# Optimization experiments

Hardware: AMD Instinct MI355X
Metric: run time of the kernel (lower is better)

The kernel has to match this reference:

```python
import jax, jax.numpy as jnp
import numpy as np

IN_FEATURES = 4096
OUT_FEATURES = 4096
SPARSITY = 0.99
NNZ = max(int(IN_FEATURES * OUT_FEATURES * (1.0 - SPARSITY)), 1)  # 167772
BATCH = 1024


def setup_inputs() -> dict:
    key = jax.random.key(0)
    kx, kv, kr, kc = jax.random.split(key, 4)
    x = jax.random.normal(kx, (BATCH, IN_FEATURES), dtype=jnp.float32)
    # values initialized ~ N(0,1) / sqrt(in_features), as in the module
    values = jax.random.normal(kv, (NNZ,), dtype=jnp.float32) * (1.0 / np.sqrt(IN_FEATURES))
    bias = jnp.zeros((OUT_FEATURES,), dtype=jnp.float32)
    rows = jax.random.randint(kr, (NNZ,), 0, IN_FEATURES)
    cols = jax.random.randint(kc, (NNZ,), 0, OUT_FEATURES)
    return {"x": x, "values": values, "bias": bias, "rows": rows, "cols": cols}


def reference(x, values, bias, rows, cols):
    # out = x @ W + bias, with sparse W(in,out) given in COO form.
    # torch's coalesce() sums duplicate (row,col) entries; scatter-add matches that.
    contrib = x[:, rows] * values  # [B, nnz]: gather input columns, scale by weights
    out = jnp.zeros((x.shape[0], OUT_FEATURES), dtype=x.dtype)
    out = out.at[:, cols].add(contrib)  # scatter-add into output columns
    return out + bias[None, :]
```

## Files before the change

kernel.cpp:

```cpp
#include <hip/hip_runtime.h>
#include <hip/hip_fp16.h>

#define BATCH 1024
#define IN_F 4096
#define OUT_F 4096
#define NCHUNK 8
#define CHUNK (BATCH / NCHUNK)
#define CAP 128

__global__ __launch_bounds__(256) void transpose_zero_k(const float* __restrict__ src,
                                                        __half* __restrict__ dst,
                                                        int R, int C,
                                                        int* __restrict__ cursor,
                                                        int4* __restrict__ rvz,
                                                        int rvz_n) {
    __shared__ float tile[32][33];
    const int tx = threadIdx.x, ty = threadIdx.y;
    const int c0 = blockIdx.x * 32, r0 = blockIdx.y * 32;
#pragma unroll
    for (int j = 0; j < 4; ++j) {
        int r = r0 + ty + j * 8;
        tile[ty + j * 8][tx] = src[(size_t)r * C + c0 + tx];
    }
    const int tid = ty * 32 + tx;
    const int gtid = (blockIdx.y * gridDim.x + blockIdx.x) * 256 + tid;
    const int nthreads = gridDim.x * gridDim.y * 256;
    if (gtid < OUT_F) cursor[gtid] = 0;
    for (int i = gtid; i < rvz_n; i += nthreads) rvz[i] = make_int4(0, 0, 0, 0);
    __syncthreads();
#pragma unroll
    for (int j = 0; j < 4; ++j) {
        int c = c0 + ty + j * 8;
        dst[(size_t)c * R + r0 + tx] = __float2half(tile[tx][ty + j * 8]);
    }
}

__global__ void scatter_k(const int* __restrict__ rows, const int* __restrict__ cols,
                          const float* __restrict__ vals, int nnz,
                          int* __restrict__ cursor, int2* __restrict__ rv) {
    int k = blockIdx.x * 256 + threadIdx.x;
    if (k < nnz) {
        int c = cols[k];
        int pos = atomicAdd(&cursor[c], 1);
        rv[(size_t)c * CAP + pos] = make_int2(rows[k], __float_as_int(vals[k]));
    }
}

__device__ inline void fma8(float acc[8], uint4 h, float v) {
    union { unsigned u; __half2 h2; } cv;
    float2 f;
    cv.u = h.x; f = __half22float2(cv.h2);
    acc[0] = fmaf(v, f.x, acc[0]); acc[1] = fmaf(v, f.y, acc[1]);
    cv.u = h.y; f = __half22float2(cv.h2);
    acc[2] = fmaf(v, f.x, acc[2]); acc[3] = fmaf(v, f.y, acc[3]);
    cv.u = h.z; f = __half22float2(cv.h2);
    acc[4] = fmaf(v, f.x, acc[4]); acc[5] = fmaf(v, f.y, acc[5]);
    cv.u = h.w; f = __half22float2(cv.h2);
    acc[6] = fmaf(v, f.x, acc[6]); acc[7] = fmaf(v, f.y, acc[7]);
}

__global__ __launch_bounds__(256, 4) void spmm_k(const __half* __restrict__ xTh,
                                                 const int* __restrict__ cursor,
                                                 const int2* __restrict__ rv,
                                                 const float* __restrict__ bias,
                                                 float* __restrict__ out) {
    __shared__ float red[4][128];
    const int chunk = blockIdx.x & (NCHUNK - 1);
    const int colBase = (blockIdx.x >> 3) * 4;
    const int w = threadIdx.x >> 6;
    const int lane = threadIdx.x & 63;
    const int q = lane >> 4;
    const int ql = lane & 15;
    const int c = __builtin_amdgcn_readfirstlane(colBase + w);

    const int groups = (cursor[c] + 7) >> 3;

    const char* __restrict__ xbase =
        (const char*)xTh + chunk * (CHUNK * 2) + ql * 16;
    const int4* __restrict__ pq = (const int4*)(rv + (size_t)c * CAP) + q;

    float acc[8] = {0, 0, 0, 0, 0, 0, 0, 0};

    int4 e = pq[0];
#pragma unroll 2
    for (int g = 0; g < groups; ++g) {
        int4 en = pq[(size_t)(g + 1) * 4];
        uint4 hA = *(const uint4*)(xbase + ((size_t)e.x << 11));
        uint4 hB = *(const uint4*)(xbase + ((size_t)e.z << 11));
        float vA = __int_as_float(e.y);
        float vB = __int_as_float(e.w);
        fma8(acc, hA, vA);
        fma8(acc, hB, vB);
        e = en;
    }

#pragma unroll
    for (int j = 0; j < 8; ++j) {
        acc[j] += __shfl_xor(acc[j], 16);
        acc[j] += __shfl_xor(acc[j], 32);
    }

    if (q == 0) {
        *(float4*)&red[w][ql * 8 + 0] = make_float4(acc[0], acc[1], acc[2], acc[3]);
        *(float4*)&red[w][ql * 8 + 4] = make_float4(acc[4], acc[5], acc[6], acc[7]);
    }
    __syncthreads();

    const int t = threadIdx.x;
    if (t < 128) {
        float4 o;
        o.x = red[0][t] + bias[colBase + 0];
        o.y = red[1][t] + bias[colBase + 1];
        o.z = red[2][t] + bias[colBase + 2];
        o.w = red[3][t] + bias[colBase + 3];
        *(float4*)(out + (size_t)(chunk * CHUNK + t) * OUT_F + colBase) = o;
    }
}

__global__ void bias_init_k(const float* __restrict__ bias, float* __restrict__ out) {
    int i = blockIdx.x * 256 + threadIdx.x;
    out[i] = bias[i & (OUT_F - 1)];
}
__global__ void fallback_k(const float* __restrict__ x, const float* __restrict__ vals,
                           const int* __restrict__ rows, const int* __restrict__ cols,
                           float* __restrict__ out) {
    int k = blockIdx.x;
    int r = rows[k], c = cols[k];
    float v = vals[k];
    for (int b = threadIdx.x; b < BATCH; b += 256)
        atomicAdd(&out[(size_t)b * OUT_F + c], v * x[(size_t)b * IN_F + r]);
}

extern "C" void kernel_launch(void* const* d_in, const int* in_sizes, int n_in,
                              void* d_out, int out_size, void* d_ws, size_t ws_size,
                              hipStream_t stream) {
    const float* x    = (const float*)d_in[0];
    const float* vals = (const float*)d_in[1];
    const float* bias = (const float*)d_in[2];
    const int*   rows = (const int*)d_in[3];
    const int*   cols = (const int*)d_in[4];
    float* out = (float*)d_out;
    const int nnz = in_sizes[1];

    const size_t rv_entries = (size_t)OUT_F * CAP;
    const size_t rv_bytes = rv_entries * 8 + 64;
    const int rvz_n = (int)(rv_bytes / 16);

    size_t off = 0;
    auto alloc = [&](size_t bytes) {
        void* p = (char*)d_ws + off;
        off += (bytes + 255) & ~(size_t)255;
        return p;
    };
    __half* xTh   = (__half*)alloc((size_t)IN_F * BATCH * 2);
    int*   cursor = (int*)alloc(OUT_F * 4);
    int2*  rv     = (int2*)alloc(rv_bytes);

    if (off > ws_size) {
        bias_init_k<<<(BATCH * OUT_F) / 256, 256, 0, stream>>>(bias, out);
        fallback_k<<<nnz, 256, 0, stream>>>(x, vals, rows, cols, out);
        return;
    }

    transpose_zero_k<<<dim3(IN_F / 32, BATCH / 32), dim3(32, 8), 0, stream>>>(
        x, xTh, BATCH, IN_F, cursor, (int4*)rv, rvz_n);
    scatter_k<<<(nnz + 255) / 256, 256, 0, stream>>>(rows, cols, vals, nnz, cursor, rv);
    spmm_k<<<(OUT_F / 4) * NCHUNK, 256, 0, stream>>>(xTh, cursor, rv, bias, out);
}
```

Before: 115.8 us.

## Fuse COO scatter into transpose kernel and drop rv buffer zeroing

Merges the scatter and the x transpose/fp16 conversion into a single launch, with scatter blocks placed first and transpose blocks after. Zeroing of the 4 MB bucket buffer goes away; cursors are now cleared with a memset, and the tail group is masked by count instead of relying on zero-filled padding. The spmm inner loop is software-pipelined so row gathers are issued one group ahead, and row indices are masked so stale entries stay in bounds. This removes one launch and a large memory write, at the cost of an extra memset call and tail-masking logic.

```diff
diff --git a/kernel.cpp b/kernel.cpp
--- a/kernel.cpp
+++ b/kernel.cpp
@@ -7,42 +7,43 @@
 #define NCHUNK 8
 #define CHUNK (BATCH / NCHUNK)
 #define CAP 128
+#define TBLK ((IN_F / 32) * (BATCH / 32))
 
-__global__ __launch_bounds__(256) void transpose_zero_k(const float* __restrict__ src,
-                                                        __half* __restrict__ dst,
-                                                        int R, int C,
-                                                        int* __restrict__ cursor,
-                                                        int4* __restrict__ rvz,
-                                                        int rvz_n) {
+__global__ __launch_bounds__(256) void prep_k(const float* __restrict__ src,
+                                              __half* __restrict__ dst,
+                                              const int* __restrict__ rows,
+                                              const int* __restrict__ cols,
+                                              const float* __restrict__ vals,
+                                              int nnz, int nscat,
+                                              int* __restrict__ cursor,
+                                              int2* __restrict__ rv) {
+    const int tid = threadIdx.x;
+    if ((int)blockIdx.x < nscat) {
+        int k = blockIdx.x * 256 + tid;
+        if (k < nnz) {
+            int c = cols[k];
+            int pos = atomicAdd(&cursor[c], 1);
+            if (pos < CAP)
+                rv[(size_t)c * CAP + pos] = make_int2(rows[k], __float_as_int(vals[k]));
+        }
+        return;
+    }
     __shared__ float tile[32][33];
-    const int tx = threadIdx.x, ty = threadIdx.y;
-    const int c0 = blockIdx.x * 32, r0 = blockIdx.y * 32;
+    const int b = blockIdx.x - nscat;
+    const int bx = b & (IN_F / 32 - 1);
+    const int by = b >> 7;
+    const int tx = tid & 31, ty = tid >> 5;
+    const int c0 = bx * 32, r0 = by * 32;
 #pragma unroll
     for (int j = 0; j < 4; ++j) {
         int r = r0 + ty + j * 8;
-        tile[ty + j * 8][tx] = src[(size_t)r * C + c0 + tx];
+        tile[ty + j * 8][tx] = src[(size_t)r * IN_F + c0 + tx];
     }
-    const int tid = ty * 32 + tx;
-    const int gtid = (blockIdx.y * gridDim.x + blockIdx.x) * 256 + tid;
-    const int nthreads = gridDim.x * gridDim.y * 256;
-    if (gtid < OUT_F) cursor[gtid] = 0;
-    for (int i = gtid; i < rvz_n; i += nthreads) rvz[i] = make_int4(0, 0, 0, 0);
     __syncthreads();
 #pragma unroll
     for (int j = 0; j < 4; ++j) {
         int c = c0 + ty + j * 8;
-        dst[(size_t)c * R + r0 + tx] = __float2half(tile[tx][ty + j * 8]);
-    }
-}
-
-__global__ void scatter_k(const int* __restrict__ rows, const int* __restrict__ cols,
-                          const float* __restrict__ vals, int nnz,
-                          int* __restrict__ cursor, int2* __restrict__ rv) {
-    int k = blockIdx.x * 256 + threadIdx.x;
-    if (k < nnz) {
-        int c = cols[k];
-        int pos = atomicAdd(&cursor[c], 1);
-        rv[(size_t)c * CAP + pos] = make_int2(rows[k], __float_as_int(vals[k]));
+        dst[(size_t)c * BATCH + r0 + tx] = __float2half(tile[tx][ty + j * 8]);
     }
 }
 
@@ -73,7 +74,10 @@
     const int ql = lane & 15;
     const int c = __builtin_amdgcn_readfirstlane(colBase + w);
 
-    const int groups = (cursor[c] + 7) >> 3;
+    int cnt = cursor[c];
+    cnt = cnt > CAP ? CAP : cnt;
+    const int gfull = cnt >> 3;
+    const int rem = cnt & 7;
 
     const char* __restrict__ xbase =
         (const char*)xTh + chunk * (CHUNK * 2) + ql * 16;
@@ -81,17 +85,26 @@
 
     float acc[8] = {0, 0, 0, 0, 0, 0, 0, 0};
 
-    int4 e = pq[0];
+    int4 e0 = pq[0];
+    uint4 hA = *(const uint4*)(xbase + ((size_t)(e0.x & (IN_F - 1)) << 11));
+    uint4 hB = *(const uint4*)(xbase + ((size_t)(e0.z & (IN_F - 1)) << 11));
+    int4 e1 = pq[4];
+
 #pragma unroll 2
-    for (int g = 0; g < groups; ++g) {
-        int4 en = pq[(size_t)(g + 1) * 4];
-        uint4 hA = *(const uint4*)(xbase + ((size_t)e.x << 11));
-        uint4 hB = *(const uint4*)(xbase + ((size_t)e.z << 11));
-        float vA = __int_as_float(e.y);
-        float vB = __int_as_float(e.w);
+    for (int g = 0; g < gfull; ++g) {
+        int4 e2 = pq[(size_t)(g + 2) * 4];
+        uint4 hA1 = *(const uint4*)(xbase + ((size_t)(e1.x & (IN_F - 1)) << 11));
+        uint4 hB1 = *(const uint4*)(xbase + ((size_t)(e1.z & (IN_F - 1)) << 11));
+        fma8(acc, hA, __int_as_float(e0.y));
+        fma8(acc, hB, __int_as_float(e0.w));
+        e0 = e1; e1 = e2; hA = hA1; hB = hB1;
+    }
+    if (rem) {
+        const int i0 = gfull * 8 + 2 * q;
+        float vA = (i0 < cnt) ? __int_as_float(e0.y) : 0.0f;
+        float vB = (i0 + 1 < cnt) ? __int_as_float(e0.w) : 0.0f;
         fma8(acc, hA, vA);
         fma8(acc, hB, vB);
-        e = en;
     }
 
 #pragma unroll
@@ -142,9 +155,7 @@
     float* out = (float*)d_out;
     const int nnz = in_sizes[1];
 
-    const size_t rv_entries = (size_t)OUT_F * CAP;
-    const size_t rv_bytes = rv_entries * 8 + 64;
-    const int rvz_n = (int)(rv_bytes / 16);
+    const size_t rv_bytes = (size_t)OUT_F * CAP * 8 + 256;
 
     size_t off = 0;
     auto alloc = [&](size_t bytes) {
@@ -162,8 +173,9 @@
         return;
     }
 
-    transpose_zero_k<<<dim3(IN_F / 32, BATCH / 32), dim3(32, 8), 0, stream>>>(
-        x, xTh, BATCH, IN_F, cursor, (int4*)rv, rvz_n);
-    scatter_k<<<(nnz + 255) / 256, 256, 0, stream>>>(rows, cols, vals, nnz, cursor, rv);
+    const int nscat = (nnz + 255) / 256;
+    hipMemsetAsync(cursor, 0, OUT_F * sizeof(int), stream);
+    prep_k<<<nscat + TBLK, 256, 0, stream>>>(x, xTh, rows, cols, vals, nnz, nscat,
+                                             cursor, rv);
     spmm_k<<<(OUT_F / 4) * NCHUNK, 256, 0, stream>>>(xTh, cursor, rv, bias, out);
 }
```

Result: faster. 112.6 us (-2.8%).
